# Kernel tuning notes

Measured on AMD Instinct MI355X. Metric: run time of the kernel, lower is better.

The kernel has to match this reference:

```python
import jax, jax.numpy as jnp
import numpy as np

N_NODES = 100000
K_HOPS = 2


def _add_self_loops(edge_index, n):
    loop = jnp.arange(n, dtype=edge_index.dtype)
    src = jnp.concatenate([edge_index[0], loop])
    dst = jnp.concatenate([edge_index[1], loop])
    return src, dst


def _gcn_norm(src, dst, n):
    # symmetric normalization D^-1/2 (A+I) D^-1/2
    deg = jax.ops.segment_sum(jnp.ones_like(dst, dtype=jnp.float32), dst, num_segments=n)
    dinv = jnp.where(deg > 0, jax.lax.rsqrt(deg), 0.0)
    return dinv[src] * dinv[dst]  # [E]


def setup_inputs() -> dict:
    key = jax.random.key(0)
    k1, k2, k3, k4, k5 = jax.random.split(key, 5)
    in_f, out_f = 128, 64
    x = jax.random.normal(k1, (N_NODES, in_f), dtype=jnp.float32)
    edge_index = jax.random.randint(k2, (2, 1600000), 0, N_NODES, dtype=jnp.int64)
    s1 = 1.0 / np.sqrt(in_f)
    W1 = jax.random.uniform(k3, (in_f, in_f), dtype=jnp.float32, minval=-s1, maxval=s1)
    b1 = jnp.zeros((in_f,), dtype=jnp.float32)
    W2 = jax.random.uniform(k4, (out_f, in_f), dtype=jnp.float32, minval=-s1, maxval=s1)
    b2 = jnp.zeros((out_f,), dtype=jnp.float32)
    return {"x": x, "edge_index": edge_index, "W1": W1, "b1": b1, "W2": W2, "b2": b2}


def reference(x, edge_index, W1, b1, W2, b2):
    n = x.shape[0]
    src, dst = _add_self_loops(edge_index, n)
    norm = _gcn_norm(src, dst, n)
    for _ in range(K_HOPS):
        msg = x[src] * norm[:, None]                      # [E+N, F] gather
        x = jax.ops.segment_sum(msg, dst, num_segments=n)  # scatter-add
    # transform: Linear -> ReLU -> Linear -> log_softmax
    h = jax.nn.relu(x @ W1.T + b1)
    logits = h @ W2.T + b2
    return jax.nn.log_softmax(logits, axis=1)
```

## Files before the change

### kernel.cpp

```cpp
#include <hip/hip_runtime.h>
#include <math.h>

#define CAP 64
#define NSLICE 256
#define SLMAX 392

typedef __attribute__((ext_vector_type(8))) short short8;
typedef __attribute__((ext_vector_type(4))) float f32x4;
typedef __attribute__((ext_vector_type(4))) int int4v;

static __device__ inline unsigned short f2bf(float f) {
    unsigned int u = __float_as_uint(f);
    u += 0x7fffu + ((u >> 16) & 1u);
    return (unsigned short)(u >> 16);
}
static __device__ inline float bf_lo(unsigned int u) { return __uint_as_float(u << 16); }
static __device__ inline float bf_hi(unsigned int u) { return __uint_as_float(u & 0xffff0000u); }
static __device__ inline unsigned int pack2(float lo, float hi) {
    return ((unsigned int)f2bf(hi) << 16) | (unsigned int)f2bf(lo);
}


__global__ __launch_bounds__(256) void part_k(
    const int* __restrict__ dst, const int* __restrict__ src, int E,
    unsigned long long mul, int qcap, int2* __restrict__ queue, int* __restrict__ qcnt,
    int gb_p,
    const float2* __restrict__ W1f, unsigned int* __restrict__ w1b, int n1,
    const float2* __restrict__ W2f, unsigned int* __restrict__ w2b, int n2)
{
    if (blockIdx.x >= gb_p) {
        int i = (blockIdx.x - gb_p) * 256 + threadIdx.x;
        if (i < n1) {
            float2 v = W1f[i];
            w1b[i] = pack2(v.x, v.y);
        } else if (i < n1 + n2) {
            float2 v = W2f[i - n1];
            w2b[i - n1] = pack2(v.x, v.y);
        }
        return;
    }

    __shared__ int lcnt[NSLICE];
    __shared__ int gbase[NSLICE];
    lcnt[threadIdx.x] = 0;
    __syncthreads();

    int base = blockIdx.x * 2048 + threadIdx.x * 8;
    int nv = E - base; nv = nv > 8 ? 8 : (nv < 0 ? 0 : nv);

    int d[8], sv[8], sl[8], lp[8];
    if (nv == 8) {
        int4v da = __builtin_nontemporal_load((const int4v*)(dst + base));
        int4v db = __builtin_nontemporal_load((const int4v*)(dst + base + 4));
        int4v sa = __builtin_nontemporal_load((const int4v*)(src + base));
        int4v sb = __builtin_nontemporal_load((const int4v*)(src + base + 4));
#pragma unroll
        for (int j = 0; j < 4; j++) {
            d[j] = da[j]; sv[j] = sa[j];
            d[4 + j] = db[j]; sv[4 + j] = sb[j];
        }
    } else {
        for (int j = 0; j < nv; j++) { d[j] = dst[base + j]; sv[j] = src[base + j]; }
    }

#pragma unroll
    for (int j = 0; j < 8; j++) {
        if (j < nv) {
            sl[j] = (int)(((unsigned long long)(unsigned)d[j] * mul) >> 40);
            lp[j] = atomicAdd(&lcnt[sl[j]], 1);
        }
    }
    __syncthreads();
    gbase[threadIdx.x] = atomicAdd(&qcnt[threadIdx.x], lcnt[threadIdx.x]);
    __syncthreads();
#pragma unroll
    for (int j = 0; j < 8; j++) {
        if (j < nv) {
            int p = gbase[sl[j]] + lp[j];
            if (p < qcap) queue[(size_t)sl[j] * qcap + p] = make_int2(d[j], sv[j]);
        }
    }
}


__global__ __launch_bounds__(256) void scat_lds_k(
    const int2* __restrict__ queue, const int* __restrict__ qcnt, int qcap,
    int sl, int n, const float4* __restrict__ x4,
    int* __restrict__ cnt, float* __restrict__ dinv,
    int* __restrict__ bkt, unsigned int* __restrict__ xb)
{
    int s  = blockIdx.x;
    int lo = s * sl;
    int hi = lo + sl < n ? lo + sl : n;
    int nn = hi - lo;
    if (nn <= 0) return;

    __shared__ int cur[SLMAX];
    __shared__ float sdv[SLMAX];
    for (int i = threadIdx.x; i < nn; i += 256) cur[i] = 0;
    __syncthreads();

    int m = qcnt[s]; if (m > qcap) m = qcap;
    const long long* __restrict__ q = (const long long*)(queue + (size_t)s * qcap);
    for (int i = threadIdx.x; i < m; i += 256) {
        long long r = __builtin_nontemporal_load(q + i);
        int d  = (int)(r & 0xffffffffll);
        int sv = (int)(r >> 32);
        int pos = atomicAdd(&cur[d - lo], 1);
        if (pos < CAP) bkt[(size_t)d * CAP + pos] = sv;
    }
    __syncthreads();
    for (int i = threadIdx.x; i < nn; i += 256) {
        int c = cur[i];
        cnt[lo + i] = c;
        float dv = rsqrtf((float)(c + 1));
        dinv[lo + i] = dv;
        sdv[i] = dv;
    }
    __syncthreads();
    for (int j = threadIdx.x; j < nn * 32; j += 256) {
        int nl = j >> 5, f4 = j & 31;
        float4 v = x4[(size_t)(lo + nl) * 32 + f4];
        float sc = sdv[nl];
        uint2 o;
        o.x = pack2(v.x * sc, v.y * sc);
        o.y = pack2(v.z * sc, v.w * sc);
        ((uint2*)xb)[(size_t)(lo + nl) * 32 + f4] = o;
    }
}


__global__ __launch_bounds__(256) void gather_b_k(
    const unsigned int* __restrict__ xin,
    const int* __restrict__ cnt, const int* __restrict__ bkt,
    const float* __restrict__ dinv,
    unsigned int* __restrict__ xout, int n)
{
    int v = blockIdx.x * 4 + (threadIdx.x >> 6);
    if (v >= n) return;
    int l = threadIdx.x & 63;
    int c = cnt[v]; if (c > CAP) c = CAP;
    c = __builtin_amdgcn_readfirstlane(c);

    int be = bkt[(size_t)v * CAP + l];
    unsigned int us = xin[(size_t)v * 64 + l];
    float ax = 0.f, ay = 0.f;

    int i = 0;
    for (; i + 16 <= c; i += 16) {
        unsigned int u[16];
#pragma unroll
        for (int j = 0; j < 16; j++) {
            int s = __builtin_amdgcn_readlane(be, i + j);
            u[j] = xin[(size_t)s * 64 + l];
        }
#pragma unroll
        for (int j = 0; j < 16; j++) { ax += bf_lo(u[j]); ay += bf_hi(u[j]); }
    }
    for (; i + 8 <= c; i += 8) {
        unsigned int u[8];
#pragma unroll
        for (int j = 0; j < 8; j++) {
            int s = __builtin_amdgcn_readlane(be, i + j);
            u[j] = xin[(size_t)s * 64 + l];
        }
#pragma unroll
        for (int j = 0; j < 8; j++) { ax += bf_lo(u[j]); ay += bf_hi(u[j]); }
    }
    for (; i + 4 <= c; i += 4) {
        unsigned int u[4];
#pragma unroll
        for (int j = 0; j < 4; j++) {
            int s = __builtin_amdgcn_readlane(be, i + j);
            u[j] = xin[(size_t)s * 64 + l];
        }
#pragma unroll
        for (int j = 0; j < 4; j++) { ax += bf_lo(u[j]); ay += bf_hi(u[j]); }
    }
    for (; i < c; i++) {
        int s = __builtin_amdgcn_readlane(be, i);
        unsigned int u = xin[(size_t)s * 64 + l];
        ax += bf_lo(u); ay += bf_hi(u);
    }

    ax += bf_lo(us);
    ay += bf_hi(us);

    float dv = dinv[v];
    float sc = dv * dv;
    xout[(size_t)v * 64 + l] = pack2(ax * sc, ay * sc);
}


__global__ __launch_bounds__(256) void gather_transform_k(
    const unsigned int* __restrict__ z1b,
    const int* __restrict__ cnt, const int* __restrict__ bkt,
    const float* __restrict__ dinv,
    const unsigned short* __restrict__ w1b, const float* __restrict__ b1,
    const unsigned short* __restrict__ w2b, const float* __restrict__ b2,
    float* __restrict__ out, int n)
{
    __shared__ __align__(16) unsigned char ldsU[64 * 304];
    unsigned int   (*X2s)[68]  = (unsigned int(*)[68])ldsU;
    unsigned short (*Hs)[152]  = (unsigned short(*)[152])ldsU;

    int t = threadIdx.x;
    int w = t >> 6;
    int l = t & 63;
    int lg = l >> 4;
    int ll = l & 15;
    int node0 = blockIdx.x * 64;

    for (int k = 0; k < 16; k++) {
        int vl = w * 16 + k;
        int v = node0 + vl;
        if (v >= n) break;
        int c = cnt[v]; if (c > CAP) c = CAP;
        c = __builtin_amdgcn_readfirstlane(c);
        int be = bkt[(size_t)v * CAP + l];
        unsigned int us = z1b[(size_t)v * 64 + l];
        float ax = 0.f, ay = 0.f;
        int i = 0;
        for (; i + 8 <= c; i += 8) {
            unsigned int u[8];
#pragma unroll
            for (int j = 0; j < 8; j++) {
                int s = __builtin_amdgcn_readlane(be, i + j);
                u[j] = z1b[(size_t)s * 64 + l];
            }
#pragma unroll
            for (int j = 0; j < 8; j++) { ax += bf_lo(u[j]); ay += bf_hi(u[j]); }
        }
        for (; i < c; i++) {
            int s = __builtin_amdgcn_readlane(be, i);
            unsigned int u = z1b[(size_t)s * 64 + l];
            ax += bf_lo(u); ay += bf_hi(u);
        }
        float dv = dinv[v];
        X2s[vl][l] = pack2((ax + bf_lo(us)) * dv, (ay + bf_hi(us)) * dv);
    }
    __syncthreads();

    short8 a[4];
#pragma unroll
    for (int kb = 0; kb < 4; kb++)
        a[kb] = *(const short8*)&X2s[w * 16 + ll][kb * 16 + lg * 4];
    __syncthreads();

    f32x4 acc[8];
#pragma unroll
    for (int nt = 0; nt < 8; nt++) {
        float bv = b1[nt * 16 + ll];
        acc[nt][0] = bv; acc[nt][1] = bv; acc[nt][2] = bv; acc[nt][3] = bv;
    }
#pragma unroll
    for (int nt = 0; nt < 8; nt++) {
        const unsigned short* wrow = w1b + (size_t)(nt * 16 + ll) * 128 + lg * 8;
#pragma unroll
        for (int kb = 0; kb < 4; kb++) {
            short8 bf = *(const short8*)(wrow + kb * 32);
            acc[nt] = __builtin_amdgcn_mfma_f32_16x16x32_bf16(a[kb], bf, acc[nt], 0, 0, 0);
        }
    }

#pragma unroll
    for (int nt = 0; nt < 8; nt++) {
#pragma unroll
        for (int r = 0; r < 4; r++) {
            float hv = fmaxf(acc[nt][r], 0.f);
            Hs[w * 16 + lg * 4 + r][nt * 16 + ll] = f2bf(hv);
        }
    }

    short8 ha[4];
#pragma unroll
    for (int kb = 0; kb < 4; kb++)
        ha[kb] = *(const short8*)&Hs[w * 16 + ll][kb * 32 + lg * 8];

    f32x4 acc2[4];
#pragma unroll
    for (int nt = 0; nt < 4; nt++) {
        float bv = b2[nt * 16 + ll];
        acc2[nt][0] = bv; acc2[nt][1] = bv; acc2[nt][2] = bv; acc2[nt][3] = bv;
        const unsigned short* wrow = w2b + (size_t)(nt * 16 + ll) * 128 + lg * 8;
#pragma unroll
        for (int kb = 0; kb < 4; kb++) {
            short8 bf = *(const short8*)(wrow + kb * 32);
            acc2[nt] = __builtin_amdgcn_mfma_f32_16x16x32_bf16(ha[kb], bf, acc2[nt], 0, 0, 0);
        }
    }

#pragma unroll
    for (int r = 0; r < 4; r++) {
        float m = fmaxf(fmaxf(acc2[0][r], acc2[1][r]), fmaxf(acc2[2][r], acc2[3][r]));
        m = fmaxf(m, __shfl_xor(m, 1));
        m = fmaxf(m, __shfl_xor(m, 2));
        m = fmaxf(m, __shfl_xor(m, 4));
        m = fmaxf(m, __shfl_xor(m, 8));
        float s = __expf(acc2[0][r] - m) + __expf(acc2[1][r] - m) +
                  __expf(acc2[2][r] - m) + __expf(acc2[3][r] - m);
        s += __shfl_xor(s, 1);
        s += __shfl_xor(s, 2);
        s += __shfl_xor(s, 4);
        s += __shfl_xor(s, 8);
        float lse = m + __logf(s);
        int node = node0 + w * 16 + lg * 4 + r;
        if (node < n) {
#pragma unroll
            for (int nt = 0; nt < 4; nt++)
                out[(size_t)node * 64 + nt * 16 + ll] = acc2[nt][r] - lse;
        }
    }
}


static inline size_t align256(size_t x) { return (x + 255) & ~(size_t)255; }

extern "C" void kernel_launch(void* const* d_in, const int* in_sizes, int n_in,
                              void* d_out, int out_size, void* d_ws, size_t ws_size,
                              hipStream_t stream) {
    const float* x  = (const float*)d_in[0];
    const int*   ei = (const int*)d_in[1];
    const float* W1 = (const float*)d_in[2];
    const float* b1 = (const float*)d_in[3];
    const float* W2 = (const float*)d_in[4];
    const float* b2 = (const float*)d_in[5];
    float* out = (float*)d_out;

    int n = in_sizes[0] / 128;
    int E = in_sizes[1] / 2;
    const int* src = ei;
    const int* dst = ei + E;

    int sl = (n + NSLICE - 1) / NSLICE;
    int qcap = sl * 32;
    unsigned long long mul = ((1ULL << 40) + (unsigned long long)sl - 1) / (unsigned long long)sl;

    char* w = (char*)d_ws;
    size_t off = 0;
    int*          cnt  = (int*)(w + off);          off += align256((size_t)n * sizeof(int));
    int*          qcnt = (int*)(w + off);          off += align256(NSLICE * sizeof(int));
    float*        dinv = (float*)(w + off);        off += align256((size_t)n * sizeof(float));
    int*          bkt  = (int*)(w + off);          off += align256((size_t)n * CAP * sizeof(int));
    size_t xb_bytes = (size_t)NSLICE * qcap * 8;
    unsigned int* xb   = (unsigned int*)(w + off); off += align256(xb_bytes);
    unsigned int* z1b  = (unsigned int*)(w + off); off += align256((size_t)n * 64 * sizeof(unsigned int));
    unsigned int* w1b  = (unsigned int*)(w + off); off += align256((size_t)128 * 64 * sizeof(unsigned int));
    unsigned int* w2b  = (unsigned int*)(w + off);
    int2* queue = (int2*)xb;

    int tb = 256;
    int gb_g = (n + 3) / 4;
    int gb_p = (E + 2047) / 2048;
    int n1 = 128 * 128 / 2, n2 = 64 * 128 / 2;
    int gb_w = (n1 + n2 + tb - 1) / tb;

    (void)hipMemsetAsync(qcnt, 0, NSLICE * sizeof(int), stream);
    part_k<<<gb_p + gb_w, tb, 0, stream>>>(dst, src, E, mul, qcap, queue, qcnt,
                                           gb_p, (const float2*)W1, w1b, n1,
                                           (const float2*)W2, w2b, n2);
    scat_lds_k<<<NSLICE, tb, 0, stream>>>(queue, qcnt, qcap, sl, n, (const float4*)x,
                                          cnt, dinv, bkt, xb);
    gather_b_k<<<gb_g, tb, 0, stream>>>(xb, cnt, bkt, dinv, z1b, n);
    gather_transform_k<<<(n + 63) / 64, tb, 0, stream>>>(
        z1b, cnt, bkt, dinv,
        (const unsigned short*)w1b, b1, (const unsigned short*)w2b, b2, out, n);
}
```

Before: 250.0 us.

## Pack partition queue entries into 32 bits and split second hop from MLP

New measurement: 226.8 us (median of 2 runs). 9.3% less time.

```diff
diff --git a/kernel.cpp b/kernel.cpp
--- a/kernel.cpp
+++ b/kernel.cpp
@@ -23,8 +23,8 @@
 
 __global__ __launch_bounds__(256) void part_k(
     const int* __restrict__ dst, const int* __restrict__ src, int E,
-    unsigned long long mul, int qcap, int2* __restrict__ queue, int* __restrict__ qcnt,
-    int gb_p,
+    unsigned long long mul, int slice_sz, int qcap,
+    unsigned int* __restrict__ queue, int* __restrict__ qcnt, int gb_p,
     const float2* __restrict__ W1f, unsigned int* __restrict__ w1b, int n1,
     const float2* __restrict__ W2f, unsigned int* __restrict__ w2b, int n2)
 {
@@ -77,14 +77,15 @@
     for (int j = 0; j < 8; j++) {
         if (j < nv) {
             int p = gbase[sl[j]] + lp[j];
-            if (p < qcap) queue[(size_t)sl[j] * qcap + p] = make_int2(d[j], sv[j]);
+            unsigned int dloc = (unsigned int)(d[j] - sl[j] * slice_sz);
+            if (p < qcap) queue[(size_t)sl[j] * qcap + p] = (dloc << 20) | (unsigned int)sv[j];
         }
     }
 }
 
 
 __global__ __launch_bounds__(256) void scat_lds_k(
-    const int2* __restrict__ queue, const int* __restrict__ qcnt, int qcap,
+    const unsigned int* __restrict__ queue, const int* __restrict__ qcnt, int qcap,
     int sl, int n, const float4* __restrict__ x4,
     int* __restrict__ cnt, float* __restrict__ dinv,
     int* __restrict__ bkt, unsigned int* __restrict__ xb)
@@ -101,13 +102,13 @@
     __syncthreads();
 
     int m = qcnt[s]; if (m > qcap) m = qcap;
-    const long long* __restrict__ q = (const long long*)(queue + (size_t)s * qcap);
+    const unsigned int* __restrict__ q = queue + (size_t)s * qcap;
     for (int i = threadIdx.x; i < m; i += 256) {
-        long long r = __builtin_nontemporal_load(q + i);
-        int d  = (int)(r & 0xffffffffll);
-        int sv = (int)(r >> 32);
-        int pos = atomicAdd(&cur[d - lo], 1);
-        if (pos < CAP) bkt[(size_t)d * CAP + pos] = sv;
+        unsigned int r = __builtin_nontemporal_load(q + i);
+        int sv   = (int)(r & 0xFFFFFu);
+        int dloc = (int)(r >> 20);
+        int pos = atomicAdd(&cur[dloc], 1);
+        if (pos < CAP) bkt[(size_t)(lo + dloc) * CAP + pos] = sv;
     }
     __syncthreads();
     for (int i = threadIdx.x; i < nn; i += 256) {
@@ -130,6 +131,7 @@
 }
 
 
+template<bool SQ>
 __global__ __launch_bounds__(256) void gather_b_k(
     const unsigned int* __restrict__ xin,
     const int* __restrict__ cnt, const int* __restrict__ bkt,
@@ -187,22 +189,19 @@
     ay += bf_hi(us);
 
     float dv = dinv[v];
-    float sc = dv * dv;
+    float sc = SQ ? dv * dv : dv;
     xout[(size_t)v * 64 + l] = pack2(ax * sc, ay * sc);
 }
 
-
-__global__ __launch_bounds__(256) void gather_transform_k(
-    const unsigned int* __restrict__ z1b,
-    const int* __restrict__ cnt, const int* __restrict__ bkt,
-    const float* __restrict__ dinv,
-    const unsigned short* __restrict__ w1b, const float* __restrict__ b1,
-    const unsigned short* __restrict__ w2b, const float* __restrict__ b2,
+__global__ __launch_bounds__(256) void transform_mfma_k(
+    const unsigned short* __restrict__ x2b,
+    const unsigned short* __restrict__ w1b,
+    const float* __restrict__ b1,
+    const unsigned short* __restrict__ w2b,
+    const float* __restrict__ b2,
     float* __restrict__ out, int n)
 {
-    __shared__ __align__(16) unsigned char ldsU[64 * 304];
-    unsigned int   (*X2s)[68]  = (unsigned int(*)[68])ldsU;
-    unsigned short (*Hs)[152]  = (unsigned short(*)[152])ldsU;
+    __shared__ __align__(16) unsigned short Hs[64][152];
 
     int t = threadIdx.x;
     int w = t >> 6;
@@ -211,41 +210,13 @@
     int ll = l & 15;
     int node0 = blockIdx.x * 64;
 
-    for (int k = 0; k < 16; k++) {
-        int vl = w * 16 + k;
-        int v = node0 + vl;
-        if (v >= n) break;
-        int c = cnt[v]; if (c > CAP) c = CAP;
-        c = __builtin_amdgcn_readfirstlane(c);
-        int be = bkt[(size_t)v * CAP + l];
-        unsigned int us = z1b[(size_t)v * 64 + l];
-        float ax = 0.f, ay = 0.f;
-        int i = 0;
-        for (; i + 8 <= c; i += 8) {
-            unsigned int u[8];
-#pragma unroll
-            for (int j = 0; j < 8; j++) {
-                int s = __builtin_amdgcn_readlane(be, i + j);
-                u[j] = z1b[(size_t)s * 64 + l];
-            }
-#pragma unroll
-            for (int j = 0; j < 8; j++) { ax += bf_lo(u[j]); ay += bf_hi(u[j]); }
-        }
-        for (; i < c; i++) {
-            int s = __builtin_amdgcn_readlane(be, i);
-            unsigned int u = z1b[(size_t)s * 64 + l];
-            ax += bf_lo(u); ay += bf_hi(u);
-        }
-        float dv = dinv[v];
-        X2s[vl][l] = pack2((ax + bf_lo(us)) * dv, (ay + bf_hi(us)) * dv);
-    }
-    __syncthreads();
-
+    int nrow = node0 + w * 16 + ll;
+    int crow = nrow < n ? nrow : (n - 1);
+    const unsigned short* xrow = x2b + (size_t)crow * 128 + lg * 8;
     short8 a[4];
 #pragma unroll
     for (int kb = 0; kb < 4; kb++)
-        a[kb] = *(const short8*)&X2s[w * 16 + ll][kb * 16 + lg * 4];
-    __syncthreads();
+        a[kb] = *(const short8*)(xrow + kb * 32);
 
     f32x4 acc[8];
 #pragma unroll
@@ -333,7 +304,7 @@
     const int* dst = ei + E;
 
     int sl = (n + NSLICE - 1) / NSLICE;
-    int qcap = sl * 32;
+    int qcap = sl * 64;
     unsigned long long mul = ((1ULL << 40) + (unsigned long long)sl - 1) / (unsigned long long)sl;
 
     char* w = (char*)d_ws;
@@ -342,12 +313,13 @@
     int*          qcnt = (int*)(w + off);          off += align256(NSLICE * sizeof(int));
     float*        dinv = (float*)(w + off);        off += align256((size_t)n * sizeof(float));
     int*          bkt  = (int*)(w + off);          off += align256((size_t)n * CAP * sizeof(int));
-    size_t xb_bytes = (size_t)NSLICE * qcap * 8;
+    size_t xb_bytes = (size_t)NSLICE * qcap * 4;
     unsigned int* xb   = (unsigned int*)(w + off); off += align256(xb_bytes);
     unsigned int* z1b  = (unsigned int*)(w + off); off += align256((size_t)n * 64 * sizeof(unsigned int));
+    unsigned int* x2b  = (unsigned int*)(w + off); off += align256((size_t)n * 64 * sizeof(unsigned int));
     unsigned int* w1b  = (unsigned int*)(w + off); off += align256((size_t)128 * 64 * sizeof(unsigned int));
     unsigned int* w2b  = (unsigned int*)(w + off);
-    int2* queue = (int2*)xb;
+    unsigned int* queue = xb;
 
     int tb = 256;
     int gb_g = (n + 3) / 4;
@@ -356,13 +328,14 @@
     int gb_w = (n1 + n2 + tb - 1) / tb;
 
     (void)hipMemsetAsync(qcnt, 0, NSLICE * sizeof(int), stream);
-    part_k<<<gb_p + gb_w, tb, 0, stream>>>(dst, src, E, mul, qcap, queue, qcnt,
+    part_k<<<gb_p + gb_w, tb, 0, stream>>>(dst, src, E, mul, sl, qcap, queue, qcnt,
                                            gb_p, (const float2*)W1, w1b, n1,
                                            (const float2*)W2, w2b, n2);
     scat_lds_k<<<NSLICE, tb, 0, stream>>>(queue, qcnt, qcap, sl, n, (const float4*)x,
                                           cnt, dinv, bkt, xb);
-    gather_b_k<<<gb_g, tb, 0, stream>>>(xb, cnt, bkt, dinv, z1b, n);
-    gather_transform_k<<<(n + 63) / 64, tb, 0, stream>>>(
-        z1b, cnt, bkt, dinv,
-        (const unsigned short*)w1b, b1, (const unsigned short*)w2b, b2, out, n);
-}
+    gather_b_k<true ><<<gb_g, tb, 0, stream>>>(xb,  cnt, bkt, dinv, z1b, n);
+    gather_b_k<false><<<gb_g, tb, 0, stream>>>(z1b, cnt, bkt, dinv, x2b, n);
+    transform_mfma_k<<<(n + 63) / 64, tb, 0, stream>>>(
+        (const unsigned short*)x2b, (const unsigned short*)w1b, b1,
+        (const unsigned short*)w2b, b2, out, n);
+}
```
